# Optimization experiments

Hardware: AMD Instinct MI355X
Metric: run time of the kernel (lower is better)

The kernel has to match this reference:

```python
import jax, jax.numpy as jnp
import numpy as np
from jax import lax

B, H, W, D_MODEL = 2, 64, 64, 96
EXPAND = 2
D_INNER = EXPAND * D_MODEL  # 192
D_STATE = 16
D_CONV = 3
DT_RANK = -(-D_MODEL // 16)  # 6 ('auto')
K = 2  # num_direction


def diagonal_order(size):
    # faithful to SCANS 'diagonal': main diag, then upper tri row-major, then lower tri
    locs = [i * size + i for i in range(size)]
    for i in range(size):
        for j in range(i + 1, size):
            locs.append(i * size + j)
    for i in range(size):
        for j in range(i):
            locs.append(i * size + j)
    return np.asarray(locs, dtype=np.int32)

_ORDER = diagonal_order(H)               # encode: gather by locs_flat
_INV_ORDER = np.argsort(_ORDER).astype(np.int32)  # decode: gather by argsort(locs_flat)


def setup_inputs():
    key = jax.random.key(0)
    ks = jax.random.split(key, 8)
    s = 0.02
    return {
        "x": jax.random.normal(ks[0], (B, H, W, D_MODEL), jnp.float32),
        "w_in": jax.random.normal(ks[1], (2 * D_INNER, D_MODEL), jnp.float32) * s,
        "conv_w": jax.random.normal(ks[2], (D_INNER, 1, D_CONV, D_CONV), jnp.float32) * 0.1,
        "conv_b": jnp.zeros((D_INNER,), jnp.float32),
        "x_proj_w": jax.random.normal(ks[3], (K, DT_RANK + 2 * D_STATE, D_INNER), jnp.float32) * s,
        "dt_w": jax.random.uniform(ks[4], (K, D_INNER, DT_RANK), jnp.float32, -(DT_RANK ** -0.5), DT_RANK ** -0.5),
        "dt_b": jax.random.uniform(ks[5], (K, D_INNER), jnp.float32, -4.6, -2.3),  # inv-softplus of dt in [~1e-2,1e-1]
        "A_logs": jnp.tile(jnp.log(jnp.arange(1, D_STATE + 1, dtype=jnp.float32))[None, :], (K * D_INNER, 1)),
        "Ds": jnp.ones((K * D_INNER,), jnp.float32),
        "ln_g": jnp.ones((D_INNER,), jnp.float32),
        "ln_b": jnp.zeros((D_INNER,), jnp.float32),
        "w_out": jax.random.normal(ks[6], (D_MODEL, D_INNER), jnp.float32) * s,
    }


def _selective_scan(xs, dts, A, Bs, Cs, Ds2, dt_bias):
    # xs, dts: (B,K,D,L); A: (K,D,N); Bs, Cs: (B,K,N,L); Ds2, dt_bias: (K,D)
    delta = jax.nn.softplus(dts + dt_bias[None, :, :, None])           # (B,K,D,L)
    dA = jnp.exp(jnp.einsum('bkdl,kdn->lbkdn', delta, A))              # (L,B,K,D,N)
    dBu = jnp.einsum('bkdl,bknl,bkdl->lbkdn', delta, Bs, xs)           # (L,B,K,D,N)
    Ct = jnp.transpose(Cs, (3, 0, 1, 2))                               # (L,B,K,N)

    h0 = jnp.zeros(dA.shape[1:], dA.dtype)                             # (B,K,D,N)

    def step(h, inp):
        a, bu, c = inp
        h = a * h + bu
        y = jnp.einsum('bkdn,bkn->bkd', h, c)
        return h, y

    _, ys = lax.scan(step, h0, (dA, dBu, Ct))                          # ys: (L,B,K,D)
    return jnp.transpose(ys, (1, 2, 3, 0)) + Ds2[None, :, :, None] * xs  # (B,K,D,L)


def reference(x, w_in, conv_w, conv_b, x_proj_w, dt_w, dt_b, A_logs, Ds, ln_g, ln_b, w_out):
    Bsz, Hh, Ww, _ = x.shape
    L = Hh * Ww
    order = jnp.asarray(_ORDER)
    inv = jnp.asarray(_INV_ORDER)

    xz = x @ w_in.T                                   # (B,H,W,2*D_INNER)
    xi, z = jnp.split(xz, 2, axis=-1)

    xc = jnp.transpose(xi, (0, 3, 1, 2))              # (B,D,H,W)
    xc = lax.conv_general_dilated(xc, conv_w, (1, 1), 'SAME',
                                  feature_group_count=D_INNER)
    xc = jax.nn.silu(xc + conv_b[None, :, None, None])

    xf = xc.reshape(Bsz, D_INNER, L)
    xs0 = xf[:, :, order]                             # diagonal-scan encode
    xs = jnp.stack([xs0, xs0[:, :, ::-1]], axis=1)    # (B,K,D,L), fwd + reversed

    x_dbl = jnp.einsum('bkdl,kcd->bkcl', xs, x_proj_w)
    dts, Bs, Cs = jnp.split(x_dbl, [DT_RANK, DT_RANK + D_STATE], axis=2)
    dts = jnp.einsum('bkrl,kdr->bkdl', dts, dt_w)

    A = -jnp.exp(A_logs).reshape(K, D_INNER, D_STATE)
    out_y = _selective_scan(xs, dts, A, Bs, Cs, Ds.reshape(K, D_INNER), dt_b)  # (B,K,D,L)

    y = out_y[:, 0] + out_y[:, 1, :, ::-1]            # un-flip reverse direction, merge
    y = y[:, :, inv]                                  # diagonal-scan decode
    y = jnp.transpose(y, (0, 2, 1)).reshape(Bsz, Hh, Ww, D_INNER)

    mu = jnp.mean(y, axis=-1, keepdims=True)
    var = jnp.var(y, axis=-1, keepdims=True)
    y = (y - mu) * lax.rsqrt(var + 1e-5) * ln_g + ln_b  # out_norm (LayerNorm)

    y = y * jax.nn.silu(z)
    return y @ w_out.T
```

## Files before the change

kernel.cpp:

```cpp
#include <hip/hip_runtime.h>
#include <math.h>

#define BB 2
#define DM 96
#define DI 192
#define DST 16
#define DRK 6
#define LL 4096
#define NCH 128
#define CT 32

__device__ __forceinline__ int inv_ord(int i, int j) {
    if (i == j) return i;
    if (j > i)  return 64 + i * 63 - (i * (i - 1)) / 2 + (j - i - 1);
    return 2080 + (i * (i - 1)) / 2 + j;
}

__device__ __forceinline__ float silu_f(float v) {
    return v / (1.f + __expf(-v));
}

__device__ __forceinline__ float softplus_f(float a) {
    return a > 20.f ? a : __logf(1.f + __expf(a));
}

__global__ __launch_bounds__(256) void k_gemm_in(const float* __restrict__ x,
                                                 const float* __restrict__ w_in,
                                                 float* __restrict__ xi,
                                                 float* __restrict__ zs) {
    __shared__ float aT[96][68];
    __shared__ float bT[96][68];
    const int tid = threadIdx.x;
    const int bm = blockIdx.x, bn = blockIdx.y;

    for (int f = tid; f < 64 * 24; f += 256) {
        int mm = f / 24, k4 = f % 24;
        float4 v = *(const float4*)(x + (size_t)(bm * 64 + mm) * 96 + k4 * 4);
        aT[k4 * 4 + 0][mm] = v.x; aT[k4 * 4 + 1][mm] = v.y;
        aT[k4 * 4 + 2][mm] = v.z; aT[k4 * 4 + 3][mm] = v.w;
    }
    for (int f = tid; f < 64 * 24; f += 256) {
        int nn = f / 24, k4 = f % 24;
        float4 v = *(const float4*)(w_in + (size_t)(bn * 64 + nn) * 96 + k4 * 4);
        bT[k4 * 4 + 0][nn] = v.x; bT[k4 * 4 + 1][nn] = v.y;
        bT[k4 * 4 + 2][nn] = v.z; bT[k4 * 4 + 3][nn] = v.w;
    }
    __syncthreads();

    const int tn = tid & 15, tm = tid >> 4;
    float acc[4][4] = {};
#pragma unroll 4
    for (int k = 0; k < 96; ++k) {
        float4 av = *(const float4*)&aT[k][tm * 4];
        float4 bv = *(const float4*)&bT[k][tn * 4];
        acc[0][0] += av.x * bv.x; acc[0][1] += av.x * bv.y; acc[0][2] += av.x * bv.z; acc[0][3] += av.x * bv.w;
        acc[1][0] += av.y * bv.x; acc[1][1] += av.y * bv.y; acc[1][2] += av.y * bv.z; acc[1][3] += av.y * bv.w;
        acc[2][0] += av.z * bv.x; acc[2][1] += av.z * bv.y; acc[2][2] += av.z * bv.z; acc[2][3] += av.z * bv.w;
        acc[3][0] += av.w * bv.x; acc[3][1] += av.w * bv.y; acc[3][2] += av.w * bv.z; acc[3][3] += av.w * bv.w;
    }

#pragma unroll
    for (int i = 0; i < 4; ++i) {
#pragma unroll
        for (int j = 0; j < 4; ++j) {
            int m = bm * 64 + tm * 4 + i;
            int n = bn * 64 + tn * 4 + j;
            float v = acc[i][j];
            if (n < DI) xi[(size_t)m * DI + n] = v;
            else        zs[(size_t)m * DI + (n - DI)] = silu_f(v);
        }
    }
}

__global__ __launch_bounds__(256) void k_conv(const float* __restrict__ xi,
                                              const float* __restrict__ cw,
                                              const float* __restrict__ cb,
                                              float* __restrict__ xs0) {
    int t = blockIdx.x * 256 + threadIdx.x;
    int c4 = t % 48;
    int p = t / 48;
    int b = p >> 12;
    int hw = p & 4095;
    int i = hw >> 6, j = hw & 63;
    int c = c4 * 4;
    float a0 = cb[c], a1 = cb[c + 1], a2 = cb[c + 2], a3 = cb[c + 3];
#pragma unroll
    for (int kh = -1; kh <= 1; ++kh) {
        int i2 = i + kh;
        if (i2 < 0 || i2 > 63) continue;
#pragma unroll
        for (int kw = -1; kw <= 1; ++kw) {
            int j2 = j + kw;
            if (j2 < 0 || j2 > 63) continue;
            float4 v = *(const float4*)(xi + ((size_t)(b << 12) + (i2 << 6) + j2) * DI + c);
            int wi = (kh + 1) * 3 + (kw + 1);
            a0 += v.x * cw[(c + 0) * 9 + wi];
            a1 += v.y * cw[(c + 1) * 9 + wi];
            a2 += v.z * cw[(c + 2) * 9 + wi];
            a3 += v.w * cw[(c + 3) * 9 + wi];
        }
    }
    a0 = silu_f(a0); a1 = silu_f(a1); a2 = silu_f(a2); a3 = silu_f(a3);
    int m = inv_ord(i, j);
    *(float4*)(xs0 + ((size_t)(b << 12) + m) * DI + c) = make_float4(a0, a1, a2, a3);
}

__global__ __launch_bounds__(512) void k_proj4(const float* __restrict__ xs0,
                                               const float* __restrict__ xpw,
                                               float* __restrict__ t) {
    __shared__ float xa[192 * 65];
    const int tid = threadIdx.x;
    const int rowbase = blockIdx.x * 64;
    const int k = blockIdx.y;

    for (int f = tid; f < 64 * 48; f += 512) {
        int r = f / 48, q4 = f % 48;
        float4 v = *(const float4*)(xs0 + (size_t)(rowbase + r) * DI + q4 * 4);
        xa[(q4 * 4 + 0) * 65 + r] = v.x;
        xa[(q4 * 4 + 1) * 65 + r] = v.y;
        xa[(q4 * 4 + 2) * 65 + r] = v.z;
        xa[(q4 * 4 + 3) * 65 + r] = v.w;
    }
    __syncthreads();

    const int w = __builtin_amdgcn_readfirstlane(tid >> 6);
    const int lane = tid & 63;
    const float* wb = xpw + (size_t)k * 38 * DI;

    float acc[5] = {};
    const float* wr[5];
#pragma unroll
    for (int jj = 0; jj < 5; ++jj) {
        int c = w * 5 + jj; if (c > 37) c = 37;
        wr[jj] = wb + (size_t)c * DI;
    }
#pragma unroll 4
    for (int q = 0; q < DI; ++q) {
        float xv = xa[q * 65 + lane];
#pragma unroll
        for (int jj = 0; jj < 5; ++jj) acc[jj] += wr[jj][q] * xv;
    }
    __syncthreads();

    float* tt = xa;
#pragma unroll
    for (int jj = 0; jj < 5; ++jj) {
        int c = w * 5 + jj;
        tt[c * 65 + lane] = acc[jj];
    }
    __syncthreads();
    for (int f = tid; f < 64 * 38; f += 512) {
        int m = f / 38, c = f % 38;
        float v = tt[c * 65 + m];
        int outc = (k == 0) ? (c < 6 ? 64 + c : c - 6)
                            : (c < 6 ? 70 + c : 26 + c);
        t[(size_t)(rowbase + m) * 80 + outc] = v;
    }
}

__global__ __launch_bounds__(256) void k_scan_a(const float* __restrict__ xs0,
                                                const float* __restrict__ t,
                                                const float* __restrict__ A_logs,
                                                const float* __restrict__ dtw,
                                                const float* __restrict__ dtb,
                                                float* __restrict__ aprodT,
                                                float* __restrict__ hendT) {
    __shared__ float ld_delta[CT][64];
    __shared__ float ld_dx[CT][64];
    __shared__ float ld_B[CT][16];
    const int tid = threadIdx.x;
    int blk = blockIdx.x;
    int c = blk & (NCH - 1);
    int rest = blk >> 7;
    int dthird = rest % 3;
    int bk = rest / 3;
    int b = bk >> 1, k = bk & 1;
    const int koffB = k ? 32 : 0;
    const int doff = 64 + 6 * k;

    if (tid < 128) {
        int r = tid >> 2, q = tid & 3;
        int gl = c * CT + r;
        int msrc = k ? (LL - 1 - gl) : gl;
        size_t rb = (size_t)(b << 12) + msrc;
        float4 v = *(const float4*)(t + rb * 80 + koffB + q * 4);
        *(float4*)&ld_B[r][q * 4] = v;
    }
    {
        int dloc = tid & 63;
        int d = dthird * 64 + dloc;
        const float* dwr = dtw + ((size_t)k * DI + d) * 6;
        float w0 = dwr[0], w1 = dwr[1], w2 = dwr[2];
        float w3 = dwr[3], w4 = dwr[4], w5 = dwr[5];
        float bias = dtb[k * DI + d];
        for (int f = tid; f < CT * 64; f += 256) {
            int r = f >> 6;
            int gl = c * CT + r;
            int msrc = k ? (LL - 1 - gl) : gl;
            size_t rb = (size_t)(b << 12) + msrc;
            const float* tr = t + rb * 80 + doff;
            float acc = bias + tr[0] * w0 + tr[1] * w1 + tr[2] * w2
                             + tr[3] * w3 + tr[4] * w4 + tr[5] * w5;
            float dl = softplus_f(acc);
            ld_delta[r][dloc] = dl;
            ld_dx[r][dloc] = dl * xs0[rb * DI + d];
        }
    }
    __syncthreads();

    const int dd = tid >> 2, ng = tid & 3;
    const int d = dthird * 64 + dd;
    float Av0, Av1, Av2, Av3;
    {
        const float* ar = A_logs + ((size_t)k * DI + d) * 16 + ng * 4;
        Av0 = -__expf(ar[0]); Av1 = -__expf(ar[1]);
        Av2 = -__expf(ar[2]); Av3 = -__expf(ar[3]);
    }
    float h0 = 0, h1 = 0, h2 = 0, h3 = 0;
    float S = 0.f;
#pragma unroll 4
    for (int l = 0; l < CT; ++l) {
        float dl = ld_delta[l][dd];
        float dx = ld_dx[l][dd];
        float4 bv = *(const float4*)&ld_B[l][ng * 4];
        float a0 = __expf(dl * Av0), a1 = __expf(dl * Av1);
        float a2 = __expf(dl * Av2), a3 = __expf(dl * Av3);
        h0 = a0 * h0 + dx * bv.x; h1 = a1 * h1 + dx * bv.y;
        h2 = a2 * h2 + dx * bv.z; h3 = a3 * h3 + dx * bv.w;
        S += dl;
    }
    float p0 = __expf(Av0 * S), p1 = __expf(Av1 * S);
    float p2 = __expf(Av2 * S), p3 = __expf(Av3 * S);
    size_t o = ((size_t)bk * 3072 + (size_t)d * 16 + ng * 4) * 128 + c;
    aprodT[o]       = p0; hendT[o]       = h0;
    aprodT[o + 128] = p1; hendT[o + 128] = h1;
    aprodT[o + 256] = p2; hendT[o + 256] = h2;
    aprodT[o + 384] = p3; hendT[o + 384] = h3;
}

__global__ __launch_bounds__(256) void k_scan_b(const float* __restrict__ aprodT,
                                                const float* __restrict__ hendT,
                                                float* __restrict__ hinit) {
    int wid = blockIdx.x * 4 + (threadIdx.x >> 6);
    int lane = threadIdx.x & 63;
    int bk = wid / 3072;
    int rr = wid - bk * 3072;
    size_t base = ((size_t)bk * 3072 + rr) * 128;

    float a0 = aprodT[base + lane];
    float h0 = hendT [base + lane];
    float a1 = aprodT[base + 64 + lane];
    float h1 = hendT [base + 64 + lane];

#pragma unroll
    for (int off = 1; off < 64; off <<= 1) {
        float ap = __shfl_up(a0, off), hp = __shfl_up(h0, off);
        if (lane >= off) { h0 = fmaf(a0, hp, h0); a0 *= ap; }
    }
    float he = __shfl_up(h0, 1);
    float hT = __shfl(h0, 63);
    if (lane == 0) he = 0.f;
    size_t ob = (size_t)bk * NCH * 3072 + rr;
    hinit[ob + (size_t)lane * 3072] = he;

#pragma unroll
    for (int off = 1; off < 64; off <<= 1) {
        float ap = __shfl_up(a1, off), hp = __shfl_up(h1, off);
        if (lane >= off) { h1 = fmaf(a1, hp, h1); a1 *= ap; }
    }
    float ae2 = __shfl_up(a1, 1), he2 = __shfl_up(h1, 1);
    if (lane == 0) { ae2 = 1.f; he2 = 0.f; }
    hinit[ob + (size_t)(lane + 64) * 3072] = fmaf(ae2, hT, he2);
}

__global__ __launch_bounds__(256) void k_scan_c(const float* __restrict__ xs0,
                                                const float* __restrict__ t,
                                                const float* __restrict__ A_logs,
                                                const float* __restrict__ dtw,
                                                const float* __restrict__ dtb,
                                                const float* __restrict__ hinit,
                                                float* __restrict__ ya,
                                                float* __restrict__ yb) {
    __shared__ float ld_delta[CT][64];
    __shared__ float ld_dx[CT][64];
    __shared__ float ld_B[CT][16];
    __shared__ float ld_C[CT][16];
    const int tid = threadIdx.x;
    int blk = blockIdx.x;
    int c = blk & (NCH - 1);
    int rest = blk >> 7;
    int dthird = rest % 3;
    int bk = rest / 3;
    int b = bk >> 1, k = bk & 1;
    const int koffB = k ? 32 : 0;
    const int doff = 64 + 6 * k;

    {
        int r = tid >> 3, q = tid & 7;
        int gl = c * CT + r;
        int msrc = k ? (LL - 1 - gl) : gl;
        size_t rb = (size_t)(b << 12) + msrc;
        float4 v = *(const float4*)(t + rb * 80 + koffB + q * 4);
        if (q < 4) *(float4*)&ld_B[r][q * 4] = v;
        else       *(float4*)&ld_C[r][(q - 4) * 4] = v;
    }
    {
        int dloc = tid & 63;
        int d = dthird * 64 + dloc;
        const float* dwr = dtw + ((size_t)k * DI + d) * 6;
        float w0 = dwr[0], w1 = dwr[1], w2 = dwr[2];
        float w3 = dwr[3], w4 = dwr[4], w5 = dwr[5];
        float bias = dtb[k * DI + d];
        for (int f = tid; f < CT * 64; f += 256) {
            int r = f >> 6;
            int gl = c * CT + r;
            int msrc = k ? (LL - 1 - gl) : gl;
            size_t rb = (size_t)(b << 12) + msrc;
            const float* tr = t + rb * 80 + doff;
            float acc = bias + tr[0] * w0 + tr[1] * w1 + tr[2] * w2
                             + tr[3] * w3 + tr[4] * w4 + tr[5] * w5;
            float dl = softplus_f(acc);
            ld_delta[r][dloc] = dl;
            ld_dx[r][dloc] = dl * xs0[rb * DI + d];
        }
    }
    __syncthreads();

    const int dd = tid >> 2, ng = tid & 3;
    const int d = dthird * 64 + dd;
    float Av0, Av1, Av2, Av3;
    {
        const float* ar = A_logs + ((size_t)k * DI + d) * 16 + ng * 4;
        Av0 = -__expf(ar[0]); Av1 = -__expf(ar[1]);
        Av2 = -__expf(ar[2]); Av3 = -__expf(ar[3]);
    }
    float h0, h1, h2, h3;
    {
        size_t o = ((size_t)bk * NCH + c) * 3072 + (size_t)d * 16 + ng * 4;
        float4 hv = *(const float4*)(hinit + o);
        h0 = hv.x; h1 = hv.y; h2 = hv.z; h3 = hv.w;
    }
    float* ydst = k ? yb : ya;
    const size_t bbase = (size_t)(b << 12);
#pragma unroll 4
    for (int l = 0; l < CT; ++l) {
        float dl = ld_delta[l][dd];
        float dx = ld_dx[l][dd];
        float4 bv = *(const float4*)&ld_B[l][ng * 4];
        float4 cv = *(const float4*)&ld_C[l][ng * 4];
        float a0 = __expf(dl * Av0), a1 = __expf(dl * Av1);
        float a2 = __expf(dl * Av2), a3 = __expf(dl * Av3);
        h0 = a0 * h0 + dx * bv.x; h1 = a1 * h1 + dx * bv.y;
        h2 = a2 * h2 + dx * bv.z; h3 = a3 * h3 + dx * bv.w;
        float p = h0 * cv.x + h1 * cv.y + h2 * cv.z + h3 * cv.w;
        p += __shfl_xor(p, 1);
        p += __shfl_xor(p, 2);
        if (ng == 0) {
            int gl = c * CT + l;
            int msrc = k ? (LL - 1 - gl) : gl;
            ydst[(bbase + msrc) * DI + d] = p;
        }
    }
}

__global__ __launch_bounds__(256) void k_out(const float* __restrict__ ya,
                                             const float* __restrict__ yb,
                                             const float* __restrict__ xs0,
                                             const float* __restrict__ Ds,
                                             const float* __restrict__ zs,
                                             const float* __restrict__ ln_g,
                                             const float* __restrict__ ln_b,
                                             const float* __restrict__ w_out,
                                             float* __restrict__ out) {
    __shared__ float lnb[16][200];
    __shared__ float bT[96][104];
    __shared__ float stat[16][2];
    const int tid = threadIdx.x;
    const int pb = blockIdx.x * 16;

    for (int f = tid; f < 16 * 48; f += 256) {
        int r = f / 48, q4 = f % 48;
        int p = pb + r;
        int b = p >> 12, pp = p & 4095;
        int m = inv_ord(pp >> 6, pp & 63);
        size_t rbase = ((size_t)(b << 12) + m) * DI + q4 * 4;
        float4 va = *(const float4*)(ya + rbase);
        float4 vb = *(const float4*)(yb + rbase);
        float4 vx = *(const float4*)(xs0 + rbase);
        float4 d0 = *(const float4*)(Ds + q4 * 4);
        float4 d1 = *(const float4*)(Ds + DI + q4 * 4);
        lnb[r][q4 * 4 + 0] = va.x + vb.x + (d0.x + d1.x) * vx.x;
        lnb[r][q4 * 4 + 1] = va.y + vb.y + (d0.y + d1.y) * vx.y;
        lnb[r][q4 * 4 + 2] = va.z + vb.z + (d0.z + d1.z) * vx.z;
        lnb[r][q4 * 4 + 3] = va.w + vb.w + (d0.w + d1.w) * vx.w;
    }
    __syncthreads();

    if (tid < 128) {
        int r = tid >> 3, sub = tid & 7;
        float s = 0.f, s2 = 0.f;
        for (int q = 0; q < 24; ++q) {
            float v = lnb[r][sub * 24 + q];
            s += v; s2 += v * v;
        }
#pragma unroll
        for (int off = 1; off < 8; off <<= 1) {
            s += __shfl_xor(s, off);
            s2 += __shfl_xor(s2, off);
        }
        if (sub == 0) {
            float mu = s * (1.f / 192.f);
            float var = s2 * (1.f / 192.f) - mu * mu;
            stat[r][0] = mu;
            stat[r][1] = rsqrtf(var + 1e-5f);
        }
    }
    __syncthreads();

    for (int f = tid; f < 16 * 48; f += 256) {
        int r = f / 48, q4 = f % 48;
        int p = pb + r;
        float4 vz = *(const float4*)(zs + (size_t)p * DI + q4 * 4);
        float4 g  = *(const float4*)(ln_g + q4 * 4);
        float4 bb = *(const float4*)(ln_b + q4 * 4);
        float mu = stat[r][0], isd = stat[r][1];
        lnb[r][q4*4+0] = ((lnb[r][q4*4+0] - mu) * isd * g.x + bb.x) * vz.x;
        lnb[r][q4*4+1] = ((lnb[r][q4*4+1] - mu) * isd * g.y + bb.y) * vz.y;
        lnb[r][q4*4+2] = ((lnb[r][q4*4+2] - mu) * isd * g.z + bb.z) * vz.z;
        lnb[r][q4*4+3] = ((lnb[r][q4*4+3] - mu) * isd * g.w + bb.w) * vz.w;
    }

    const int tn = tid & 15, tm = tid >> 4;
    float acc[6] = {};
#pragma unroll
    for (int kt = 0; kt < 2; ++kt) {
        __syncthreads();
        for (int f = tid; f < 96 * 24; f += 256) {
            int nn = f / 24, k4 = f % 24;
            float4 v = *(const float4*)(w_out + (size_t)nn * DI + kt * 96 + k4 * 4);
            bT[k4 * 4 + 0][nn] = v.x; bT[k4 * 4 + 1][nn] = v.y;
            bT[k4 * 4 + 2][nn] = v.z; bT[k4 * 4 + 3][nn] = v.w;
        }
        __syncthreads();
#pragma unroll 4
        for (int kq = 0; kq < 96; ++kq) {
            float av = lnb[tm][kt * 96 + kq];
            float2 b0 = *(const float2*)&bT[kq][tn * 6];
            float2 b1 = *(const float2*)&bT[kq][tn * 6 + 2];
            float2 b2 = *(const float2*)&bT[kq][tn * 6 + 4];
            acc[0] += av * b0.x; acc[1] += av * b0.y;
            acc[2] += av * b1.x; acc[3] += av * b1.y;
            acc[4] += av * b2.x; acc[5] += av * b2.y;
        }
    }
    int p = pb + tm;
#pragma unroll
    for (int j = 0; j < 6; ++j)
        out[(size_t)p * DM + tn * 6 + j] = acc[j];
}

extern "C" void kernel_launch(void* const* d_in, const int* in_sizes, int n_in,
                              void* d_out, int out_size, void* d_ws, size_t ws_size,
                              hipStream_t stream) {
    (void)in_sizes; (void)n_in; (void)out_size; (void)ws_size;
    const float* x      = (const float*)d_in[0];
    const float* w_in   = (const float*)d_in[1];
    const float* conv_w = (const float*)d_in[2];
    const float* conv_b = (const float*)d_in[3];
    const float* xpw    = (const float*)d_in[4];
    const float* dtw    = (const float*)d_in[5];
    const float* dtb    = (const float*)d_in[6];
    const float* A_logs = (const float*)d_in[7];
    const float* Ds     = (const float*)d_in[8];
    const float* ln_g   = (const float*)d_in[9];
    const float* ln_b   = (const float*)d_in[10];
    const float* w_out  = (const float*)d_in[11];
    float* out = (float*)d_out;

    float* ws    = (float*)d_ws;
    float* xi    = ws;
    float* zs    = xi + 1572864;
    float* xs0   = zs + 1572864;
    float* tbuf  = xs0 + 1572864;
    float* aprod = tbuf + 1048576;
    float* hend  = aprod + 1572864;
    float* hinit = hend + 1572864;
    float* ya    = hinit + 1572864;
    float* yb    = ya + 1572864;

    k_gemm_in<<<dim3(128, 6), 256, 0, stream>>>(x, w_in, xi, zs);
    k_conv<<<1536, 256, 0, stream>>>(xi, conv_w, conv_b, xs0);
    k_proj4<<<dim3(128, 2), 512, 0, stream>>>(xs0, xpw, tbuf);
    k_scan_a<<<4 * 3 * NCH, 256, 0, stream>>>(xs0, tbuf, A_logs, dtw, dtb, aprod, hend);
    k_scan_b<<<3072, 256, 0, stream>>>(aprod, hend, hinit);
    k_scan_c<<<4 * 3 * NCH, 256, 0, stream>>>(xs0, tbuf, A_logs, dtw, dtb, hinit, ya, yb);
    k_out<<<512, 256, 0, stream>>>(ya, yb, xs0, Ds, zs, ln_g, ln_b, w_out, out);
}
```

Before: 144.4 us.

## Move chunk-state transpose into scan_b via LDS and split proj channel halves

scan_a now writes chunk products and end states as contiguous float4 rows instead of scattered transposed stores. scan_b stages 16 rows across all 128 chunks in shared memory, runs the wave prefix scans from there, and writes hinit in transposed layout. scan_c then reads four strided scalars instead of one float4. Separately, the x_proj kernel is split into two channel halves with 256-thread blocks, doubling the block count but loading the input tile twice.

```diff
diff --git a/kernel.cpp b/kernel.cpp
--- a/kernel.cpp
+++ b/kernel.cpp
@@ -105,15 +105,16 @@
     *(float4*)(xs0 + ((size_t)(b << 12) + m) * DI + c) = make_float4(a0, a1, a2, a3);
 }
 
-__global__ __launch_bounds__(512) void k_proj4(const float* __restrict__ xs0,
+__global__ __launch_bounds__(256) void k_proj5(const float* __restrict__ xs0,
                                                const float* __restrict__ xpw,
                                                float* __restrict__ t) {
     __shared__ float xa[192 * 65];
     const int tid = threadIdx.x;
     const int rowbase = blockIdx.x * 64;
-    const int k = blockIdx.y;
-
-    for (int f = tid; f < 64 * 48; f += 512) {
+    const int k = blockIdx.y >> 1;
+    const int chhalf = blockIdx.y & 1;
+
+    for (int f = tid; f < 64 * 48; f += 256) {
         int r = f / 48, q4 = f % 48;
         float4 v = *(const float4*)(xs0 + (size_t)(rowbase + r) * DI + q4 * 4);
         xa[(q4 * 4 + 0) * 65 + r] = v.x;
@@ -125,13 +126,14 @@
 
     const int w = __builtin_amdgcn_readfirstlane(tid >> 6);
     const int lane = tid & 63;
+    const int chbase = chhalf * 19 + w * 5;
     const float* wb = xpw + (size_t)k * 38 * DI;
 
     float acc[5] = {};
     const float* wr[5];
 #pragma unroll
     for (int jj = 0; jj < 5; ++jj) {
-        int c = w * 5 + jj; if (c > 37) c = 37;
+        int c = chbase + jj; if (c > 37) c = 37;
         wr[jj] = wb + (size_t)c * DI;
     }
 #pragma unroll 4
@@ -145,13 +147,14 @@
     float* tt = xa;
 #pragma unroll
     for (int jj = 0; jj < 5; ++jj) {
-        int c = w * 5 + jj;
-        tt[c * 65 + lane] = acc[jj];
-    }
-    __syncthreads();
-    for (int f = tid; f < 64 * 38; f += 512) {
-        int m = f / 38, c = f % 38;
-        float v = tt[c * 65 + m];
+        int cl = w * 5 + jj;
+        tt[cl * 65 + lane] = acc[jj];
+    }
+    __syncthreads();
+    for (int f = tid; f < 64 * 19; f += 256) {
+        int m = f / 19, cl = f % 19;
+        int c = chhalf * 19 + cl;
+        float v = tt[cl * 65 + m];
         int outc = (k == 0) ? (c < 6 ? 64 + c : c - 6)
                             : (c < 6 ? 70 + c : 26 + c);
         t[(size_t)(rowbase + m) * 80 + outc] = v;
@@ -163,8 +166,8 @@
                                                 const float* __restrict__ A_logs,
                                                 const float* __restrict__ dtw,
                                                 const float* __restrict__ dtb,
-                                                float* __restrict__ aprodT,
-                                                float* __restrict__ hendT) {
+                                                float* __restrict__ aprod,
+                                                float* __restrict__ hend) {
     __shared__ float ld_delta[CT][64];
     __shared__ float ld_dx[CT][64];
     __shared__ float ld_B[CT][16];
@@ -231,46 +234,51 @@
     }
     float p0 = __expf(Av0 * S), p1 = __expf(Av1 * S);
     float p2 = __expf(Av2 * S), p3 = __expf(Av3 * S);
-    size_t o = ((size_t)bk * 3072 + (size_t)d * 16 + ng * 4) * 128 + c;
-    aprodT[o]       = p0; hendT[o]       = h0;
-    aprodT[o + 128] = p1; hendT[o + 128] = h1;
-    aprodT[o + 256] = p2; hendT[o + 256] = h2;
-    aprodT[o + 384] = p3; hendT[o + 384] = h3;
-}
-
-__global__ __launch_bounds__(256) void k_scan_b(const float* __restrict__ aprodT,
-                                                const float* __restrict__ hendT,
-                                                float* __restrict__ hinit) {
-    int wid = blockIdx.x * 4 + (threadIdx.x >> 6);
-    int lane = threadIdx.x & 63;
-    int bk = wid / 3072;
-    int rr = wid - bk * 3072;
-    size_t base = ((size_t)bk * 3072 + rr) * 128;
-
-    float a0 = aprodT[base + lane];
-    float h0 = hendT [base + lane];
-    float a1 = aprodT[base + 64 + lane];
-    float h1 = hendT [base + 64 + lane];
-
-#pragma unroll
-    for (int off = 1; off < 64; off <<= 1) {
-        float ap = __shfl_up(a0, off), hp = __shfl_up(h0, off);
-        if (lane >= off) { h0 = fmaf(a0, hp, h0); a0 *= ap; }
-    }
-    float he = __shfl_up(h0, 1);
-    float hT = __shfl(h0, 63);
-    if (lane == 0) he = 0.f;
-    size_t ob = (size_t)bk * NCH * 3072 + rr;
-    hinit[ob + (size_t)lane * 3072] = he;
-
-#pragma unroll
-    for (int off = 1; off < 64; off <<= 1) {
-        float ap = __shfl_up(a1, off), hp = __shfl_up(h1, off);
-        if (lane >= off) { h1 = fmaf(a1, hp, h1); a1 *= ap; }
-    }
-    float ae2 = __shfl_up(a1, 1), he2 = __shfl_up(h1, 1);
-    if (lane == 0) { ae2 = 1.f; he2 = 0.f; }
-    hinit[ob + (size_t)(lane + 64) * 3072] = fmaf(ae2, hT, he2);
+    size_t o = ((size_t)bk * NCH + c) * 3072 + (size_t)d * 16 + ng * 4;
+    *(float4*)(aprod + o) = make_float4(p0, p1, p2, p3);
+    *(float4*)(hend + o)  = make_float4(h0, h1, h2, h3);
+}
+
+__global__ __launch_bounds__(256) void k_scan_b(const float* __restrict__ aprod,
+                                                const float* __restrict__ hend,
+                                                float* __restrict__ hinitT) {
+    __shared__ float la[128][17];
+    __shared__ float lh[128][17];
+    const int tid = threadIdx.x;
+    int bk = blockIdx.x / 192;
+    int rg = blockIdx.x - bk * 192;
+    size_t abase = (size_t)bk * NCH * 3072 + rg * 16;
+
+    for (int f = tid; f < 128 * 16; f += 256) {
+        int c = f >> 4, r = f & 15;
+        la[c][r] = aprod[abase + (size_t)c * 3072 + r];
+        lh[c][r] = hend [abase + (size_t)c * 3072 + r];
+    }
+    __syncthreads();
+
+    const int w = tid >> 6, lane = tid & 63;
+    size_t obase = ((size_t)bk * 3072 + rg * 16) * 128;
+    for (int rr = w; rr < 16; rr += 4) {
+        float a0 = la[lane][rr],      h0 = lh[lane][rr];
+        float a1 = la[lane + 64][rr], h1 = lh[lane + 64][rr];
+#pragma unroll
+        for (int off = 1; off < 64; off <<= 1) {
+            float ap = __shfl_up(a0, off), hp = __shfl_up(h0, off);
+            if (lane >= off) { h0 = fmaf(a0, hp, h0); a0 *= ap; }
+        }
+        float he = __shfl_up(h0, 1);
+        float hT = __shfl(h0, 63);
+        if (lane == 0) he = 0.f;
+        hinitT[obase + (size_t)rr * 128 + lane] = he;
+#pragma unroll
+        for (int off = 1; off < 64; off <<= 1) {
+            float ap = __shfl_up(a1, off), hp = __shfl_up(h1, off);
+            if (lane >= off) { h1 = fmaf(a1, hp, h1); a1 *= ap; }
+        }
+        float ae2 = __shfl_up(a1, 1), he2 = __shfl_up(h1, 1);
+        if (lane == 0) { ae2 = 1.f; he2 = 0.f; }
+        hinitT[obase + (size_t)rr * 128 + 64 + lane] = fmaf(ae2, hT, he2);
+    }
 }
 
 __global__ __launch_bounds__(256) void k_scan_c(const float* __restrict__ xs0,
@@ -278,7 +286,7 @@
                                                 const float* __restrict__ A_logs,
                                                 const float* __restrict__ dtw,
                                                 const float* __restrict__ dtb,
-                                                const float* __restrict__ hinit,
+                                                const float* __restrict__ hinitT,
                                                 float* __restrict__ ya,
                                                 float* __restrict__ yb) {
     __shared__ float ld_delta[CT][64];
@@ -336,9 +344,11 @@
     }
     float h0, h1, h2, h3;
     {
-        size_t o = ((size_t)bk * NCH + c) * 3072 + (size_t)d * 16 + ng * 4;
-        float4 hv = *(const float4*)(hinit + o);
-        h0 = hv.x; h1 = hv.y; h2 = hv.z; h3 = hv.w;
+        size_t o = ((size_t)bk * 3072 + (size_t)d * 16 + ng * 4) * 128 + c;
+        h0 = hinitT[o];
+        h1 = hinitT[o + 128];
+        h2 = hinitT[o + 256];
+        h3 = hinitT[o + 384];
     }
     float* ydst = k ? yb : ya;
     const size_t bbase = (size_t)(b << 12);
@@ -484,15 +494,15 @@
     float* tbuf  = xs0 + 1572864;
     float* aprod = tbuf + 1048576;
     float* hend  = aprod + 1572864;
-    float* hinit = hend + 1572864;
-    float* ya    = hinit + 1572864;
+    float* hinitT= hend + 1572864;
+    float* ya    = hinitT + 1572864;
     float* yb    = ya + 1572864;
 
     k_gemm_in<<<dim3(128, 6), 256, 0, stream>>>(x, w_in, xi, zs);
     k_conv<<<1536, 256, 0, stream>>>(xi, conv_w, conv_b, xs0);
-    k_proj4<<<dim3(128, 2), 512, 0, stream>>>(xs0, xpw, tbuf);
+    k_proj5<<<dim3(128, 4), 256, 0, stream>>>(xs0, xpw, tbuf);
     k_scan_a<<<4 * 3 * NCH, 256, 0, stream>>>(xs0, tbuf, A_logs, dtw, dtb, aprod, hend);
-    k_scan_b<<<3072, 256, 0, stream>>>(aprod, hend, hinit);
-    k_scan_c<<<4 * 3 * NCH, 256, 0, stream>>>(xs0, tbuf, A_logs, dtw, dtb, hinit, ya, yb);
+    k_scan_b<<<4 * 192, 256, 0, stream>>>(aprod, hend, hinitT);
+    k_scan_c<<<4 * 3 * NCH, 256, 0, stream>>>(xs0, tbuf, A_logs, dtw, dtb, hinitT, ya, yb);
     k_out<<<512, 256, 0, stream>>>(ya, yb, xs0, Ds, zs, ln_g, ln_b, w_out, out);
 }
```

After: 130.8 us. 1.1x faster.
